# Optimization experiments

Measured on AMD Instinct MI355X. Metric: run time of the kernel, lower is better.

## Reference

```python
import jax, jax.numpy as jnp
import numpy as np
from jax import lax

B, C, T = 4, 512, 2304
H = 16
D = C // H          # 32 head dim
WIN = 19            # window_size
WOV = WIN // 2      # window_overlap = 9
W = 2 * WOV + 1     # band width = 19
EPS = 1e-5          # nn.LayerNorm default eps


def _dwconv(x, w):
    # depthwise Conv1d, kernel 3, pad 1, no bias, groups=C. x:[B,C,T], w:[C,1,3]
    return lax.conv_general_dilated(x, w, (1,), ((1, 1),),
                                    dimension_numbers=('NCH', 'OIH', 'NCH'),
                                    feature_group_count=C)


def _ln_c(x, g, b):
    # LayerNorm over channel dim of [B,C,T] (torch: permute->LN(n_embd)->permute)
    m = jnp.mean(x, axis=1, keepdims=True)
    v = jnp.var(x, axis=1, keepdims=True)
    return (x - m) * lax.rsqrt(v + EPS) * g[None, :, None] + b[None, :, None]


def _pw(x, w, b):
    # 1x1 Conv1d: [B,C,T] x [O,C] -> [B,O,T]
    return jnp.einsum('oc,bct->bot', w, x) + b[None, :, None]


def setup_inputs() -> dict:
    key = jax.random.key(0)
    ks = jax.random.split(key, 10)
    s = lambda shape, k, fan: jax.random.normal(k, shape, jnp.float32) * (1.0 / np.sqrt(fan))
    inp = {
        'x': jax.random.normal(ks[0], (B, C, T), jnp.float32),
        'w_qconv': s((C, 1, 3), ks[1], 3),
        'w_kconv': s((C, 1, 3), ks[2], 3),
        'w_vconv': s((C, 1, 3), ks[3], 3),
        'g_q': jnp.ones((C,), jnp.float32), 'b_q': jnp.zeros((C,), jnp.float32),
        'g_k': jnp.ones((C,), jnp.float32), 'b_k': jnp.zeros((C,), jnp.float32),
        'g_v': jnp.ones((C,), jnp.float32), 'b_v': jnp.zeros((C,), jnp.float32),
        'w_query': s((C, C), ks[4], C), 'b_query': jnp.zeros((C,), jnp.float32),
        'w_key': s((C, C), ks[5], C), 'b_key': jnp.zeros((C,), jnp.float32),
        'w_value': s((C, C), ks[6], C), 'b_value': jnp.zeros((C,), jnp.float32),
        'w_proj': s((C, C), ks[7], C), 'b_proj': jnp.zeros((C,), jnp.float32),
    }
    # realistic variable-length padding mask (valid prefix per sequence)
    lengths = jax.random.randint(ks[8], (B,), T // 2, T + 1)
    inp['mask'] = jnp.arange(T)[None, :] < lengths[:, None]  # [B,T] bool
    return inp


def reference(x, mask, w_qconv, w_kconv, w_vconv, g_q, b_q, g_k, b_k, g_v, b_v,
              w_query, b_query, w_key, b_key, w_value, b_value, w_proj, b_proj):
    mf = mask.astype(x.dtype)[:, None, :]  # [B,1,T]
    # depthwise conv QKV (+ mask) -> LayerNorm -> 1x1 projection
    q = _pw(_ln_c(_dwconv(x, w_qconv) * mf, g_q, b_q), w_query, b_query)
    k = _pw(_ln_c(_dwconv(x, w_kconv) * mf, g_k, b_k), w_key, b_key)
    v = _pw(_ln_c(_dwconv(x, w_vconv) * mf, g_v, b_v), w_value, b_value)
    # split heads: [B,C,T] -> [B,H,T,D] (channel layout C = H*D)
    split = lambda t: t.reshape(B, H, D, T).transpose(0, 1, 3, 2)
    q, k, v = split(q), split(k), split(v)
    scale = 1.0 / np.sqrt(D)
    # banded sliding-window attention: key position for (t, j) is t + j - WOV
    idx = jnp.arange(T)[:, None] + jnp.arange(W)[None, :]  # [T,W] indices into padded axis
    pad4 = lambda t: jnp.pad(t, ((0, 0), (0, 0), (WOV, WOV), (0, 0)))
    kg = pad4(k)[:, :, idx, :]  # [B,H,T,W,D]
    vg = pad4(v)[:, :, idx, :]  # [B,H,T,W,D]
    scores = jnp.einsum('bhtd,bhtwd->bhtw', q, kg) * scale  # [B,H,T,W]
    valid = (idx >= WOV) & (idx < T + WOV)  # in-range key positions [T,W]
    keym = jnp.pad(mask, ((0, 0), (WOV, WOV)))[:, idx]  # [B,T,W] kv padding mask
    addm = jnp.where(keym, 0.0, -1e4).astype(x.dtype)[:, None]  # additive -1e4 like torch
    scores = jnp.where(valid[None, None], scores + addm, -jnp.inf)
    probs = jax.nn.softmax(scores, axis=-1)
    probs = jnp.where(mask[:, None, :, None], probs, 0.0)  # zero masked query rows
    out = jnp.einsum('bhtw,bhtwd->bhtd', probs, vg)  # [B,H,T,D]
    out = out.transpose(0, 1, 3, 2).reshape(B, C, T)
    out = _pw(out, w_proj, b_proj) * mf
    return out, mask
```

## Files before the change

kernel.cpp:

```cpp
#include <hip/hip_runtime.h>
#include <hip/hip_bf16.h>
#include <cstdint>
#include <cstddef>

#define TB 4
#define TC 512
#define TT 2304
#define TH 16
#define TD 32
#define TW 19
#define WOVR 9
#define EPSLN 1e-5f
#define SCALE 0.17677669529663687f
#define MTOT (TB * TT)
#define KSZ  512

typedef __attribute__((ext_vector_type(8))) short s16x8;
typedef __attribute__((ext_vector_type(8))) unsigned short u16x8;
typedef __attribute__((ext_vector_type(4))) float f32x4;

__device__ __forceinline__ float bf2f(unsigned short u) {
  union { unsigned int i; float f; } x; x.i = ((unsigned int)u) << 16; return x.f;
}
__device__ __forceinline__ unsigned short f2bf(float f) {
  union { __hip_bfloat16 h; unsigned short u; } c;
  c.h = __float2bfloat16(f);
  return c.u;
}
__device__ __forceinline__ void gload16(const void* g, void* l) {
  __builtin_amdgcn_global_load_lds(
      (const __attribute__((address_space(1))) unsigned int*)g,
      (__attribute__((address_space(3))) unsigned int*)l, 16, 0, 0);
}
__device__ __forceinline__ float mval(const unsigned char* mraw, int idx) {
  const uint32_t w0 = *(const uint32_t*)mraw;
  bool on;
  if (w0 == 1u)                 on = ((const int*)mraw)[idx] != 0;
  else if (w0 == 0x01010101u)   on = mraw[idx] != 0;
  else                          on = ((const float*)mraw)[idx] != 0.0f;
  return on ? 1.0f : 0.0f;
}

__global__ __launch_bounds__(512) void k_conv_ln_t(
    const float* __restrict__ x,
    const float* __restrict__ wq, const float* __restrict__ wk, const float* __restrict__ wv,
    const float* __restrict__ gq, const float* __restrict__ bq,
    const float* __restrict__ gk, const float* __restrict__ bk,
    const float* __restrict__ gv, const float* __restrict__ bv,
    const float* __restrict__ wquery, const float* __restrict__ wkey,
    const float* __restrict__ wvalue, const float* __restrict__ wproj,
    const unsigned char* __restrict__ mraw,
    unsigned short* __restrict__ Wbf, float* __restrict__ mf,
    float* __restrict__ outtail, unsigned short* __restrict__ Aall) {
  const int b = blockIdx.y;
  const int t0 = blockIdx.x * 16;
  const int tid = threadIdx.x;
  const int tt = tid & 15, cg = tid >> 4;

  {
    const int gtid = (b * 144 + blockIdx.x) * 512 + tid;
    #pragma unroll
    for (int rep = 0; rep < 4; rep++) {
      const int j = gtid + rep * 294912;
      if (j < 4 * TC * TC) {
        const int zz = j >> 18, r = j & (TC * TC - 1);
        const float* src = (zz == 0) ? wquery : (zz == 1) ? wkey
                          : (zz == 2) ? wvalue : wproj;
        Wbf[j] = f2bf(src[r]);
      }
    }
    if (gtid < TB * TT) {
      const float v = mval(mraw, gtid);
      mf[gtid] = v;
      outtail[(size_t)TB * TC * TT + gtid] = v;
    }
  }

  __shared__ float4 wlds[3][544];
  __shared__ float2 gblds[3][544];
  __shared__ float ps[3][32][17], ps2[3][32][17];
  __shared__ float mean_s[3][16], rstd_s[3][16];

  {
    const int c = tid, cp = c + (c >> 4);
    wlds[0][cp] = make_float4(wq[c*3], wq[c*3+1], wq[c*3+2], 0.f);
    wlds[1][cp] = make_float4(wk[c*3], wk[c*3+1], wk[c*3+2], 0.f);
    wlds[2][cp] = make_float4(wv[c*3], wv[c*3+1], wv[c*3+2], 0.f);
    gblds[0][cp] = make_float2(gq[c], bq[c]);
    gblds[1][cp] = make_float2(gk[c], bk[c]);
    gblds[2][cp] = make_float2(gv[c], bv[c]);
  }
  __syncthreads();

  const int tg = t0 + tt;
  const float m = mval(mraw, b * TT + tg);
  const int tm = tg > 0 ? tg - 1 : 0;
  const int tp = tg < TT - 1 ? tg + 1 : TT - 1;
  const float zl = (tg > 0) ? 1.f : 0.f;
  const float zr = (tg < TT - 1) ? 1.f : 0.f;

  const float* xb = x + ((size_t)(b * TC + cg * 16)) * TT;
  float xm[16], x0[16], xp[16];
  #pragma unroll
  for (int i = 0; i < 16; i++) {
    const float* xc = xb + (size_t)i * TT;
    xm[i] = xc[tm]; x0[i] = xc[tg]; xp[i] = xc[tp];
  }

  float s[3] = {}, s2[3] = {};
  unsigned int yp[3][8];
  #pragma unroll
  for (int i = 0; i < 16; i++) {
    const int cp = cg * 17 + i;
    const float xml = xm[i] * zl, xpl = xp[i] * zr;
    #pragma unroll
    for (int z = 0; z < 3; z++) {
      const float4 w = wlds[z][cp];
      const float y = (w.x * xml + w.y * x0[i] + w.z * xpl) * m;
      s[z] += y; s2[z] += y * y;
      const unsigned int h = f2bf(y);
      if ((i & 1) == 0) yp[z][i >> 1] = h;
      else              yp[z][i >> 1] |= h << 16;
    }
  }
  #pragma unroll
  for (int z = 0; z < 3; z++) {
    ps[z][cg][tt] = s[z]; ps2[z][cg][tt] = s2[z];
  }
  __syncthreads();
  if (tid < 48) {
    const int z = tid >> 4, tl = tid & 15;
    float su = 0.f, su2 = 0.f;
    #pragma unroll
    for (int g = 0; g < 32; g++) { su += ps[z][g][tl]; su2 += ps2[z][g][tl]; }
    const float mean = su * (1.f / TC);
    const float var  = su2 * (1.f / TC) - mean * mean;
    mean_s[z][tl] = mean;
    rstd_s[z][tl] = rsqrtf(fmaxf(var, 0.f) + EPSLN);
  }
  __syncthreads();

  #pragma unroll
  for (int z = 0; z < 3; z++) {
    const float mean = mean_s[z][tt], rs = rstd_s[z][tt];
    unsigned short tmp[16];
    #pragma unroll
    for (int i = 0; i < 16; i++) {
      const float2 gb = gblds[z][cg * 17 + i];
      const unsigned short hb = (unsigned short)(
          (i & 1) ? (yp[z][i >> 1] >> 16) : (yp[z][i >> 1] & 0xffffu));
      tmp[i] = f2bf((bf2f(hb) - mean) * rs * gb.x + gb.y);
    }
    unsigned short* oz = Aall + ((size_t)z * MTOT + b * TT + tg) * TC + cg * 16;
    *(u16x8*)(oz)     = *(const u16x8*)(tmp);
    *(u16x8*)(oz + 8) = *(const u16x8*)(tmp + 8);
  }
}

template<int F32OUT>
__global__ __launch_bounds__(256) void k_gemm_mfma(
    const unsigned short* __restrict__ Abase, const unsigned short* __restrict__ Wbase,
    const float* __restrict__ bq, const float* __restrict__ bk, const float* __restrict__ bv,
    unsigned short* __restrict__ obf, float* __restrict__ of32,
    const float* __restrict__ mf) {
  const int nw = gridDim.x;
  int w = blockIdx.x;
  w = (w & 7) * (nw >> 3) + (w >> 3);
  const int z = w / 288;
  const int rem = w - z * 288;
  const int m0 = (rem >> 2) * 128;
  const int n0 = (rem & 3) * 128;

  const unsigned short* A = Abase + (size_t)z * MTOT * KSZ;
  const unsigned short* W = Wbase + (size_t)z * KSZ * KSZ;
  const float* bias = (z == 0) ? bq : (z == 1) ? bk : bv;

  __shared__ __align__(16) unsigned short smem[6 * 4096];
  const int tid = threadIdx.x;
  const int l = tid & 63, l15 = l & 15, l4 = l >> 4;
  const int wid = tid >> 6, wm = wid >> 1, wn = wid & 1;

  const int r0 = tid >> 2;
  const int c0 = (tid & 3) ^ ((r0 >> 1) & 3);
  const int r1 = r0 + 64;
  const int c1 = (tid & 3) ^ ((r1 >> 1) & 3);
  const size_t gaA0 = (size_t)(m0 + r0) * KSZ + c0 * 8;
  const size_t gaA1 = (size_t)(m0 + r1) * KSZ + c1 * 8;
  const size_t gaB0 = (size_t)(n0 + r0) * KSZ + c0 * 8;
  const size_t gaB1 = (size_t)(n0 + r1) * KSZ + c1 * 8;

  int offA[4], offB[4];
  #pragma unroll
  for (int i = 0; i < 4; i++) {
    const int ra = wm * 64 + i * 16 + l15;
    offA[i] = (ra * 4 + (l4 ^ ((ra >> 1) & 3))) * 8;
    const int rb = wn * 64 + i * 16 + l15;
    offB[i] = (rb * 4 + (l4 ^ ((rb >> 1) & 3))) * 8;
  }

  #define STAGE(buf, kk)                                           \
    do {                                                           \
      unsigned short* Ad = smem + (buf) * 4096;                    \
      unsigned short* Bd = smem + 3 * 4096 + (buf) * 4096;         \
      gload16(A + gaA0 + (kk), Ad + tid * 8);                      \
      gload16(A + gaA1 + (kk), Ad + (tid + 256) * 8);              \
      gload16(W + gaB0 + (kk), Bd + tid * 8);                      \
      gload16(W + gaB1 + (kk), Bd + (tid + 256) * 8);              \
    } while (0)

  f32x4 acc[4][4] = {};
  STAGE(0, 0);
  STAGE(1, 32);
  asm volatile("s_waitcnt vmcnt(4)\ns_barrier" ::: "memory");

  #pragma unroll
  for (int t = 0; t < 16; ++t) {
    if (t + 2 < 16) STAGE((t + 2) % 3, (t + 2) * 32);
    const unsigned short* Ac = smem + (t % 3) * 4096;
    const unsigned short* Bc = smem + 3 * 4096 + (t % 3) * 4096;
    s16x8 av[4], bw[4];
    #pragma unroll
    for (int i = 0; i < 4; i++) {
      av[i] = *(const s16x8*)(Ac + offA[i]);
      bw[i] = *(const s16x8*)(Bc + offB[i]);
    }
    __builtin_amdgcn_s_setprio(1);
    #pragma unroll
    for (int mi = 0; mi < 4; mi++)
      #pragma unroll
      for (int nj = 0; nj < 4; nj++)
        acc[mi][nj] = __builtin_amdgcn_mfma_f32_16x16x32_bf16(
            bw[nj], av[mi], acc[mi][nj], 0, 0, 0);
    __builtin_amdgcn_s_setprio(0);
    if (t < 14)
      asm volatile("s_waitcnt vmcnt(4) lgkmcnt(0)\ns_barrier" ::: "memory");
    else if (t == 14)
      asm volatile("s_waitcnt vmcnt(0) lgkmcnt(0)\ns_barrier" ::: "memory");
  }
  #undef STAGE

  if (!F32OUT) {
    unsigned short* O = obf + (size_t)z * MTOT * KSZ;
    #pragma unroll
    for (int nj = 0; nj < 4; nj++) {
      const int ch0 = n0 + wn * 64 + nj * 16 + l4 * 4;
      const float4 bi = *(const float4*)&bias[ch0];
      #pragma unroll
      for (int mi = 0; mi < 4; mi++) {
        const int bt = m0 + wm * 64 + mi * 16 + l15;
        uint2 pk;
        pk.x = (uint32_t)f2bf(acc[mi][nj][0] + bi.x) |
               ((uint32_t)f2bf(acc[mi][nj][1] + bi.y) << 16);
        pk.y = (uint32_t)f2bf(acc[mi][nj][2] + bi.z) |
               ((uint32_t)f2bf(acc[mi][nj][3] + bi.w) << 16);
        *(uint2*)&O[(size_t)bt * KSZ + ch0] = pk;
      }
    }
  } else {
    const int bb = m0 / TT;
    const int tl0 = m0 - bb * TT;
    #pragma unroll
    for (int mi = 0; mi < 4; mi++) {
      const int bt = m0 + wm * 64 + mi * 16 + l15;
      const int tloc = tl0 + wm * 64 + mi * 16 + l15;
      const float mm = mf[bt];
      #pragma unroll
      for (int nj = 0; nj < 4; nj++) {
        const int ch0 = n0 + wn * 64 + nj * 16 + l4 * 4;
        const float4 bi = *(const float4*)&bias[ch0];
        #pragma unroll
        for (int r = 0; r < 4; r++) {
          const float biv = r == 0 ? bi.x : r == 1 ? bi.y : r == 2 ? bi.z : bi.w;
          of32[((size_t)(bb * TC + ch0 + r)) * TT + tloc] =
              (acc[mi][nj][r] + biv) * mm;
        }
      }
    }
  }
}

#define AROWS (128 + 2 * WOVR)
#define ASTR  36
__global__ __launch_bounds__(256) void k_attn_lds(
    const unsigned short* __restrict__ QKV, const float* __restrict__ mf,
    unsigned short* __restrict__ AO) {
  const int t0 = blockIdx.x * 128;
  const int h = blockIdx.y, b = blockIdx.z;
  const int tid = threadIdx.x;
  const int tloc = tid >> 1, half = tid & 1;
  const size_t SZ = (size_t)MTOT * KSZ;
  const unsigned short* Qp = QKV;
  const unsigned short* Kp = QKV + SZ;
  const unsigned short* Vp = QKV + 2 * SZ;
  __shared__ unsigned short Ks[AROWS * ASTR], Vs[AROWS * ASTR];
  __shared__ float mfs[AROWS];

  for (int idx = tid; idx < 2 * AROWS * 4; idx += 256) {
    const int bufv = idx >= AROWS * 4;
    const int ci = idx - bufv * AROWS * 4;
    const int r = ci >> 2, c = ci & 3;
    const int tk = t0 - WOVR + r;
    const int tkc = tk < 0 ? 0 : (tk >= TT ? TT - 1 : tk);
    const unsigned short* src =
        (bufv ? Vp : Kp) + ((size_t)(b * TT + tkc)) * TC + h * TD + c * 8;
    uint4 v = *(const uint4*)src;
    unsigned short* dst = (bufv ? Vs : Ks) + r * ASTR + c * 8;
    uint2 lo; lo.x = v.x; lo.y = v.y;
    uint2 hi; hi.x = v.z; hi.y = v.w;
    *(uint2*)dst = lo; *(uint2*)(dst + 4) = hi;
  }
  if (tid < AROWS) {
    const int tk = t0 - WOVR + tid;
    mfs[tid] = (tk >= 0 && tk < TT) ? (mf[b * TT + tk] != 0.f ? 0.f : -1e4f)
                                    : -1e30f;
  }
  __syncthreads();

  const int t = t0 + tloc;
  const float qm = mf[b * TT + t];
  float q[16];
  {
    const unsigned short* qr = Qp + ((size_t)(b * TT + t)) * TC + h * TD + half * 16;
    #pragma unroll
    for (int c = 0; c < 2; c++) {
      u16x8 v = *(const u16x8*)(qr + c * 8);
      #pragma unroll
      for (int j = 0; j < 8; j++) q[c * 8 + j] = bf2f(v[j]);
    }
  }
  float e[TW];
  float smax = -3.0e38f;
  #pragma unroll
  for (int j = 0; j < TW; j++) {
    const unsigned short* kr = Ks + (tloc + j) * ASTR + half * 16;
    float acc = 0.f;
    #pragma unroll
    for (int c = 0; c < 4; c++) {
      uint2 w = *(const uint2*)(kr + c * 4);
      acc = fmaf(q[c*4+0], bf2f((unsigned short)(w.x & 0xffffu)), acc);
      acc = fmaf(q[c*4+1], bf2f((unsigned short)(w.x >> 16)), acc);
      acc = fmaf(q[c*4+2], bf2f((unsigned short)(w.y & 0xffffu)), acc);
      acc = fmaf(q[c*4+3], bf2f((unsigned short)(w.y >> 16)), acc);
    }
    acc += __shfl_xor(acc, 1, 64);
    const float sv = acc * SCALE + mfs[tloc + j];
    e[j] = sv;
    smax = fmaxf(smax, sv);
  }
  float den = 0.f;
  #pragma unroll
  for (int j = 0; j < TW; j++) { const float ev = __expf(e[j] - smax); e[j] = ev; den += ev; }
  float o[16] = {};
  #pragma unroll
  for (int j = 0; j < TW; j++) {
    const unsigned short* vr = Vs + (tloc + j) * ASTR + half * 16;
    const float p = e[j];
    #pragma unroll
    for (int c = 0; c < 4; c++) {
      uint2 w = *(const uint2*)(vr + c * 4);
      o[c*4+0] = fmaf(p, bf2f((unsigned short)(w.x & 0xffffu)), o[c*4+0]);
      o[c*4+1] = fmaf(p, bf2f((unsigned short)(w.x >> 16)), o[c*4+1]);
      o[c*4+2] = fmaf(p, bf2f((unsigned short)(w.y & 0xffffu)), o[c*4+2]);
      o[c*4+3] = fmaf(p, bf2f((unsigned short)(w.y >> 16)), o[c*4+3]);
    }
  }
  const float sc = qm / den;
  unsigned short tmp[16];
  #pragma unroll
  for (int i = 0; i < 16; i++) tmp[i] = f2bf(o[i] * sc);
  unsigned short* op = AO + ((size_t)(b * TT + t)) * TC + h * TD + half * 16;
  *(u16x8*)(op)     = *(const u16x8*)(tmp);
  *(u16x8*)(op + 8) = *(const u16x8*)(tmp + 8);
}

extern "C" void kernel_launch(void* const* d_in, const int* in_sizes, int n_in,
                              void* d_out, int out_size, void* d_ws, size_t ws_size,
                              hipStream_t stream) {
  const float* x       = (const float*)d_in[0];
  const float* w_qconv = (const float*)d_in[1];
  const float* w_kconv = (const float*)d_in[2];
  const float* w_vconv = (const float*)d_in[3];
  const float* g_q = (const float*)d_in[4];
  const float* b_q = (const float*)d_in[5];
  const float* g_k = (const float*)d_in[6];
  const float* b_k = (const float*)d_in[7];
  const float* g_v = (const float*)d_in[8];
  const float* b_v = (const float*)d_in[9];
  const float* w_query = (const float*)d_in[10];
  const float* b_query = (const float*)d_in[11];
  const float* w_key   = (const float*)d_in[12];
  const float* b_key   = (const float*)d_in[13];
  const float* w_value = (const float*)d_in[14];
  const float* b_value = (const float*)d_in[15];
  const float* w_proj  = (const float*)d_in[16];
  const float* b_proj  = (const float*)d_in[17];
  const unsigned char* mraw = (const unsigned char*)d_in[18];
  float* out = (float*)d_out;

  uint8_t* w8 = (uint8_t*)d_ws;
  float* mf            = (float*)w8;
  unsigned short* Wbf  = (unsigned short*)(w8 + (1ull << 20));
  unsigned short* Aall = (unsigned short*)(w8 + (4ull << 20));
  unsigned short* QKV  = (unsigned short*)(w8 + (34ull << 20));
  unsigned short* AO   = (unsigned short*)(w8 + (63ull << 20));

  k_conv_ln_t<<<dim3(144, TB), dim3(512), 0, stream>>>(
      x, w_qconv, w_kconv, w_vconv, g_q, b_q, g_k, b_k, g_v, b_v,
      w_query, w_key, w_value, w_proj, mraw, Wbf, mf, out, Aall);
  k_gemm_mfma<0><<<dim3(864), dim3(256), 0, stream>>>(
      Aall, Wbf, b_query, b_key, b_value, QKV, nullptr, mf);
  k_attn_lds<<<dim3(TT / 128, TH, TB), dim3(256), 0, stream>>>(QKV, mf, AO);
  k_gemm_mfma<1><<<dim3(288), dim3(256), 0, stream>>>(
      AO, Wbf + 3 * TC * TC, b_proj, b_proj, b_proj, nullptr, out, mf);
}
```

Measured before the change: 90.08 us.

## Load GEMM operands directly into registers instead of staging through LDS

Replaces the LDS triple-buffered global_load_lds pipeline in the MFMA GEMM with per-wave direct global loads of the fragments into registers, double-buffered across k-steps. This removes the LDS writes and reads and the per-iteration barriers. In exchange, each wave reloads A and B rows that neighbouring waves also use, increasing global and L2 traffic, and the strided 16-byte loads may coalesce poorly.

```diff
diff --git a/kernel.cpp b/kernel.cpp
--- a/kernel.cpp
+++ b/kernel.cpp
@@ -26,11 +26,6 @@
   union { __hip_bfloat16 h; unsigned short u; } c;
   c.h = __float2bfloat16(f);
   return c.u;
-}
-__device__ __forceinline__ void gload16(const void* g, void* l) {
-  __builtin_amdgcn_global_load_lds(
-      (const __attribute__((address_space(1))) unsigned int*)g,
-      (__attribute__((address_space(3))) unsigned int*)l, 16, 0, 0);
 }
 __device__ __forceinline__ float mval(const unsigned char* mraw, int idx) {
   const uint32_t w0 = *(const uint32_t*)mraw;
@@ -158,7 +153,7 @@
 }
 
 template<int F32OUT>
-__global__ __launch_bounds__(256) void k_gemm_mfma(
+__global__ __launch_bounds__(256) void k_gemm_reg(
     const unsigned short* __restrict__ Abase, const unsigned short* __restrict__ Wbase,
     const float* __restrict__ bq, const float* __restrict__ bk, const float* __restrict__ bv,
     unsigned short* __restrict__ obf, float* __restrict__ of32,
@@ -175,54 +170,34 @@
   const unsigned short* W = Wbase + (size_t)z * KSZ * KSZ;
   const float* bias = (z == 0) ? bq : (z == 1) ? bk : bv;
 
-  __shared__ __align__(16) unsigned short smem[6 * 4096];
   const int tid = threadIdx.x;
   const int l = tid & 63, l15 = l & 15, l4 = l >> 4;
   const int wid = tid >> 6, wm = wid >> 1, wn = wid & 1;
 
-  const int r0 = tid >> 2;
-  const int c0 = (tid & 3) ^ ((r0 >> 1) & 3);
-  const int r1 = r0 + 64;
-  const int c1 = (tid & 3) ^ ((r1 >> 1) & 3);
-  const size_t gaA0 = (size_t)(m0 + r0) * KSZ + c0 * 8;
-  const size_t gaA1 = (size_t)(m0 + r1) * KSZ + c1 * 8;
-  const size_t gaB0 = (size_t)(n0 + r0) * KSZ + c0 * 8;
-  const size_t gaB1 = (size_t)(n0 + r1) * KSZ + c1 * 8;
-
-  int offA[4], offB[4];
+  const unsigned short* pa[4];
+  const unsigned short* pb[4];
   #pragma unroll
   for (int i = 0; i < 4; i++) {
-    const int ra = wm * 64 + i * 16 + l15;
-    offA[i] = (ra * 4 + (l4 ^ ((ra >> 1) & 3))) * 8;
-    const int rb = wn * 64 + i * 16 + l15;
-    offB[i] = (rb * 4 + (l4 ^ ((rb >> 1) & 3))) * 8;
-  }
-
-  #define STAGE(buf, kk)                                           \
-    do {                                                           \
-      unsigned short* Ad = smem + (buf) * 4096;                    \
-      unsigned short* Bd = smem + 3 * 4096 + (buf) * 4096;         \
-      gload16(A + gaA0 + (kk), Ad + tid * 8);                      \
-      gload16(A + gaA1 + (kk), Ad + (tid + 256) * 8);              \
-      gload16(W + gaB0 + (kk), Bd + tid * 8);                      \
-      gload16(W + gaB1 + (kk), Bd + (tid + 256) * 8);              \
-    } while (0)
+    pa[i] = A + (size_t)(m0 + wm * 64 + i * 16 + l15) * KSZ + l4 * 8;
+    pb[i] = W + (size_t)(n0 + wn * 64 + i * 16 + l15) * KSZ + l4 * 8;
+  }
 
   f32x4 acc[4][4] = {};
-  STAGE(0, 0);
-  STAGE(1, 32);
-  asm volatile("s_waitcnt vmcnt(4)\ns_barrier" ::: "memory");
-
+  s16x8 av[2][4], bw[2][4];
+  #pragma unroll
+  for (int i = 0; i < 4; i++) {
+    av[0][i] = *(const s16x8*)(pa[i]);
+    bw[0][i] = *(const s16x8*)(pb[i]);
+  }
   #pragma unroll
   for (int t = 0; t < 16; ++t) {
-    if (t + 2 < 16) STAGE((t + 2) % 3, (t + 2) * 32);
-    const unsigned short* Ac = smem + (t % 3) * 4096;
-    const unsigned short* Bc = smem + 3 * 4096 + (t % 3) * 4096;
-    s16x8 av[4], bw[4];
-    #pragma unroll
-    for (int i = 0; i < 4; i++) {
-      av[i] = *(const s16x8*)(Ac + offA[i]);
-      bw[i] = *(const s16x8*)(Bc + offB[i]);
+    const int cur = t & 1, nxt = cur ^ 1;
+    if (t + 1 < 16) {
+      #pragma unroll
+      for (int i = 0; i < 4; i++) {
+        av[nxt][i] = *(const s16x8*)(pa[i] + (t + 1) * 32);
+        bw[nxt][i] = *(const s16x8*)(pb[i] + (t + 1) * 32);
+      }
     }
     __builtin_amdgcn_s_setprio(1);
     #pragma unroll
@@ -230,14 +205,9 @@
       #pragma unroll
       for (int nj = 0; nj < 4; nj++)
         acc[mi][nj] = __builtin_amdgcn_mfma_f32_16x16x32_bf16(
-            bw[nj], av[mi], acc[mi][nj], 0, 0, 0);
+            bw[cur][nj], av[cur][mi], acc[mi][nj], 0, 0, 0);
     __builtin_amdgcn_s_setprio(0);
-    if (t < 14)
-      asm volatile("s_waitcnt vmcnt(4) lgkmcnt(0)\ns_barrier" ::: "memory");
-    else if (t == 14)
-      asm volatile("s_waitcnt vmcnt(0) lgkmcnt(0)\ns_barrier" ::: "memory");
-  }
-  #undef STAGE
+  }
 
   if (!F32OUT) {
     unsigned short* O = obf + (size_t)z * MTOT * KSZ;
@@ -407,9 +377,9 @@
   k_conv_ln_t<<<dim3(144, TB), dim3(512), 0, stream>>>(
       x, w_qconv, w_kconv, w_vconv, g_q, b_q, g_k, b_k, g_v, b_v,
       w_query, w_key, w_value, w_proj, mraw, Wbf, mf, out, Aall);
-  k_gemm_mfma<0><<<dim3(864), dim3(256), 0, stream>>>(
+  k_gemm_reg<0><<<dim3(864), dim3(256), 0, stream>>>(
       Aall, Wbf, b_query, b_key, b_value, QKV, nullptr, mf);
   k_attn_lds<<<dim3(TT / 128, TH, TB), dim3(256), 0, stream>>>(QKV, mf, AO);
-  k_gemm_mfma<1><<<dim3(288), dim3(256), 0, stream>>>(
+  k_gemm_reg<1><<<dim3(288), dim3(256), 0, stream>>>(
       AO, Wbf + 3 * TC * TC, b_proj, b_proj, b_proj, nullptr, out, mf);
 }
```

After: 150.1 us. 1.67x slower.

## Load x rows coalesced per channel and transpose conv output through LDS

Applied to the files above, without the earlier changes.

The prologue kernel previously had each thread gather 16 channels at one time step, which made strided global loads. Now each thread owns one channel, reads 16 consecutive time steps with float4 loads plus two halo values, and computes the depthwise conv for q, k and v in registers. Each result is transposed through a shared-memory buffer so LayerNorm statistics and the bf16 output keep the channel-contiguous layout. The cost is a per-z loop with several extra barriers and a 32 KB LDS tile. LayerNorm now uses the fp32 conv values rather than bf16-rounded ones.

```diff
diff --git a/kernel.cpp b/kernel.cpp
--- a/kernel.cpp
+++ b/kernel.cpp
@@ -76,84 +76,85 @@
     }
   }
 
-  __shared__ float4 wlds[3][544];
+  __shared__ float ys[512][16];
+  __shared__ float ps[32][17], ps2[32][17];
+  __shared__ float mean_s[16], rstd_s[16];
   __shared__ float2 gblds[3][544];
-  __shared__ float ps[3][32][17], ps2[3][32][17];
-  __shared__ float mean_s[3][16], rstd_s[3][16];
 
   {
     const int c = tid, cp = c + (c >> 4);
-    wlds[0][cp] = make_float4(wq[c*3], wq[c*3+1], wq[c*3+2], 0.f);
-    wlds[1][cp] = make_float4(wk[c*3], wk[c*3+1], wk[c*3+2], 0.f);
-    wlds[2][cp] = make_float4(wv[c*3], wv[c*3+1], wv[c*3+2], 0.f);
     gblds[0][cp] = make_float2(gq[c], bq[c]);
     gblds[1][cp] = make_float2(gk[c], bk[c]);
     gblds[2][cp] = make_float2(gv[c], bv[c]);
   }
-  __syncthreads();
-
-  const int tg = t0 + tt;
-  const float m = mval(mraw, b * TT + tg);
-  const int tm = tg > 0 ? tg - 1 : 0;
-  const int tp = tg < TT - 1 ? tg + 1 : TT - 1;
-  const float zl = (tg > 0) ? 1.f : 0.f;
-  const float zr = (tg < TT - 1) ? 1.f : 0.f;
-
-  const float* xb = x + ((size_t)(b * TC + cg * 16)) * TT;
-  float xm[16], x0[16], xp[16];
-  #pragma unroll
-  for (int i = 0; i < 16; i++) {
-    const float* xc = xb + (size_t)i * TT;
-    xm[i] = xc[tm]; x0[i] = xc[tg]; xp[i] = xc[tp];
-  }
-
-  float s[3] = {}, s2[3] = {};
-  unsigned int yp[3][8];
-  #pragma unroll
-  for (int i = 0; i < 16; i++) {
-    const int cp = cg * 17 + i;
-    const float xml = xm[i] * zl, xpl = xp[i] * zr;
-    #pragma unroll
-    for (int z = 0; z < 3; z++) {
-      const float4 w = wlds[z][cp];
-      const float y = (w.x * xml + w.y * x0[i] + w.z * xpl) * m;
-      s[z] += y; s2[z] += y * y;
-      const unsigned int h = f2bf(y);
-      if ((i & 1) == 0) yp[z][i >> 1] = h;
-      else              yp[z][i >> 1] |= h << 16;
-    }
-  }
-  #pragma unroll
+
+  const float* xc = x + ((size_t)(b * TC + tid)) * TT;
+  float xr[18];
+  {
+    const float4 v0 = *(const float4*)&xc[t0];
+    const float4 v1 = *(const float4*)&xc[t0 + 4];
+    const float4 v2 = *(const float4*)&xc[t0 + 8];
+    const float4 v3 = *(const float4*)&xc[t0 + 12];
+    xr[1] = v0.x;  xr[2] = v0.y;  xr[3] = v0.z;  xr[4] = v0.w;
+    xr[5] = v1.x;  xr[6] = v1.y;  xr[7] = v1.z;  xr[8] = v1.w;
+    xr[9] = v2.x;  xr[10] = v2.y; xr[11] = v2.z; xr[12] = v2.w;
+    xr[13] = v3.x; xr[14] = v3.y; xr[15] = v3.z; xr[16] = v3.w;
+    xr[0]  = (t0 > 0)       ? xc[t0 - 1]  : 0.f;
+    xr[17] = (t0 + 16 < TT) ? xc[t0 + 16] : 0.f;
+  }
+  float mk[16];
+  #pragma unroll
+  for (int j = 0; j < 16; j++) mk[j] = mval(mraw, b * TT + t0 + j);
+  float wcv[3][3];
+  #pragma unroll
+  for (int k = 0; k < 3; k++) {
+    wcv[0][k] = wq[tid * 3 + k];
+    wcv[1][k] = wk[tid * 3 + k];
+    wcv[2][k] = wv[tid * 3 + k];
+  }
+
   for (int z = 0; z < 3; z++) {
-    ps[z][cg][tt] = s[z]; ps2[z][cg][tt] = s2[z];
-  }
-  __syncthreads();
-  if (tid < 48) {
-    const int z = tid >> 4, tl = tid & 15;
-    float su = 0.f, su2 = 0.f;
-    #pragma unroll
-    for (int g = 0; g < 32; g++) { su += ps[z][g][tl]; su2 += ps2[z][g][tl]; }
-    const float mean = su * (1.f / TC);
-    const float var  = su2 * (1.f / TC) - mean * mean;
-    mean_s[z][tl] = mean;
-    rstd_s[z][tl] = rsqrtf(fmaxf(var, 0.f) + EPSLN);
-  }
-  __syncthreads();
-
-  #pragma unroll
-  for (int z = 0; z < 3; z++) {
-    const float mean = mean_s[z][tt], rs = rstd_s[z][tt];
+    float y[16];
+    #pragma unroll
+    for (int j = 0; j < 16; j++)
+      y[j] = (wcv[z][0] * xr[j] + wcv[z][1] * xr[j + 1] +
+              wcv[z][2] * xr[j + 2]) * mk[j];
+    #pragma unroll
+    for (int q = 0; q < 4; q++)
+      *(float4*)&ys[tid][q * 4] =
+          make_float4(y[q * 4], y[q * 4 + 1], y[q * 4 + 2], y[q * 4 + 3]);
+    __syncthreads();
+    float yv[16], su = 0.f, su2 = 0.f;
+    #pragma unroll
+    for (int i = 0; i < 16; i++) {
+      const float v = ys[cg * 16 + i][tt];
+      yv[i] = v; su += v; su2 += v * v;
+    }
+    ps[cg][tt] = su; ps2[cg][tt] = su2;
+    __syncthreads();
+    if (tid < 16) {
+      float s1 = 0.f, s2 = 0.f;
+      #pragma unroll
+      for (int g = 0; g < 32; g++) { s1 += ps[g][tid]; s2 += ps2[g][tid]; }
+      const float mean = s1 * (1.f / TC);
+      const float var  = s2 * (1.f / TC) - mean * mean;
+      mean_s[tid] = mean;
+      rstd_s[tid] = rsqrtf(fmaxf(var, 0.f) + EPSLN);
+    }
+    __syncthreads();
+    const float mean = mean_s[tt], rs = rstd_s[tt];
     unsigned short tmp[16];
     #pragma unroll
     for (int i = 0; i < 16; i++) {
-      const float2 gb = gblds[z][cg * 17 + i];
-      const unsigned short hb = (unsigned short)(
-          (i & 1) ? (yp[z][i >> 1] >> 16) : (yp[z][i >> 1] & 0xffffu));
-      tmp[i] = f2bf((bf2f(hb) - mean) * rs * gb.x + gb.y);
-    }
-    unsigned short* oz = Aall + ((size_t)z * MTOT + b * TT + tg) * TC + cg * 16;
+      const int c = cg * 16 + i;
+      const float2 gb = gblds[z][c + (c >> 4)];
+      tmp[i] = f2bf((yv[i] - mean) * rs * gb.x + gb.y);
+    }
+    unsigned short* oz =
+        Aall + ((size_t)z * MTOT + b * TT + t0 + tt) * TC + cg * 16;
     *(u16x8*)(oz)     = *(const u16x8*)(tmp);
     *(u16x8*)(oz + 8) = *(const u16x8*)(tmp + 8);
+    __syncthreads();
   }
 }
 
```

Result: slower. 97.20 us (+7.9%).
